# Kernel optimization log

Measured on AMD Instinct MI355X. Metric: run time of the kernel, lower is better.

The kernel has to match this reference:

```python
import jax, jax.numpy as jnp
import numpy as np

N_QUBITS = 12
N_LAYERS = 3
STATE_DIM = 2 ** N_QUBITS  # 4096


def _cnot_perms():
    # Ring of CNOTs: control q -> target (q+1) % n. Qubit 0 is the MSB of the basis index.
    idx = np.arange(STATE_DIM)
    perms = []
    for c in range(N_QUBITS):
        t = (c + 1) % N_QUBITS
        cbit = (idx >> (N_QUBITS - 1 - c)) & 1
        perms.append(np.where(cbit == 1, idx ^ (1 << (N_QUBITS - 1 - t)), idx))
    return np.stack(perms)  # (n_qubits, STATE_DIM), each row an involutive permutation

_CNOT = _cnot_perms()


def _z_signs():
    # sign_q(i) = +1 if bit q of basis index i is 0, else -1
    idx = np.arange(STATE_DIM)
    bits = (idx[None, :] >> (N_QUBITS - 1 - np.arange(N_QUBITS)[:, None])) & 1
    return (1.0 - 2.0 * bits).astype(np.float32)  # (n_qubits, STATE_DIM)

_ZSIGN = jnp.asarray(_z_signs())


def _apply_ry(s, th, q):
    # RY(th) on qubit q, batched over leading dim. RY is real so the state stays real.
    L, R = 2 ** q, 2 ** (N_QUBITS - 1 - q)
    s = s.reshape(-1, L, 2, R)
    c, sn = jnp.cos(th / 2), jnp.sin(th / 2)
    a0 = c * s[:, :, 0, :] - sn * s[:, :, 1, :]
    a1 = sn * s[:, :, 0, :] + c * s[:, :, 1, :]
    return jnp.stack([a0, a1], axis=2).reshape(-1, STATE_DIM)


def _quantum_features(xr, theta):
    # Amplitude encoding: normalize each row to a unit state vector.
    s = xr / (jnp.linalg.norm(xr, axis=1, keepdims=True) + 1e-10)
    for l in range(N_LAYERS):
        for q in range(N_QUBITS):
            s = _apply_ry(s, theta[l, q], q)
        for q in range(N_QUBITS):
            s = s[:, _CNOT[q]]  # CNOT as a static gather permutation
    probs = s * s  # |amplitude|^2 (real state)
    return probs @ _ZSIGN.T  # (B, n_qubits) Pauli-Z expectations


def setup_inputs() -> dict:
    key = jax.random.key(0)
    ks = jax.random.split(key, 9)
    B, F = 8192, 8192
    d = {}
    d["x"] = jax.random.normal(ks[0], (B, F), jnp.float32)
    # feature reducer Linear(F, STATE_DIM)
    d["W_red"] = jax.random.normal(ks[1], (STATE_DIM, F), jnp.float32) / np.sqrt(F).astype(np.float32)
    d["b_red"] = jnp.zeros((STATE_DIM,), jnp.float32)
    # variational RY angles
    d["theta"] = jax.random.normal(ks[2], (N_LAYERS, N_QUBITS), jnp.float32)
    # classical head: n_qubits -> 32 -> 16 -> 1
    d["W1"] = jax.random.normal(ks[3], (32, N_QUBITS), jnp.float32) / np.sqrt(N_QUBITS).astype(np.float32)
    d["b1"] = jnp.zeros((32,), jnp.float32)
    d["W2"] = jax.random.normal(ks[4], (16, 32), jnp.float32) / np.sqrt(32.0).astype(np.float32)
    d["b2"] = jnp.zeros((16,), jnp.float32)
    d["W3"] = jax.random.normal(ks[5], (1, 16), jnp.float32) / 4.0
    d["b3"] = jnp.zeros((1,), jnp.float32)
    return d


def reference(x, W_red, b_red, theta, W1, b1, W2, b2, W3, b3):
    xr = x @ W_red.T + b_red                      # (B, STATE_DIM)
    m = _quantum_features(xr, theta)              # (B, N_QUBITS)
    h = jax.nn.relu(m @ W1.T + b1)                # dropout is identity at inference
    h = jax.nn.relu(h @ W2.T + b2)
    return jax.nn.sigmoid(h @ W3.T + b3)          # (B, 1) risk scores
```

## Files before the change

kernel.cpp:

```cpp
#include <hip/hip_runtime.h>
#include <hip/hip_bf16.h>

#define NQ    12
#define SDIM  4096
#define BATCH 8192
#define FDIM  8192

using bf16x8 = __attribute__((ext_vector_type(8))) short;
using f16x8  = __attribute__((ext_vector_type(8))) _Float16;
using f32x4  = __attribute__((ext_vector_type(4))) float;

__device__ __forceinline__ unsigned short f2bf(float f) {
    unsigned u = __float_as_uint(f);
    u += 0x7FFFu + ((u >> 16) & 1u);
    return (unsigned short)(u >> 16);
}
__device__ __forceinline__ float bf2f(unsigned short h) {
    return __uint_as_float(((unsigned)h) << 16);
}

__device__ __forceinline__ void gl_lds16(const void* g, void* l) {
    __builtin_amdgcn_global_load_lds(
        (const __attribute__((address_space(1))) void*)g,
        (__attribute__((address_space(3))) void*)l, 16, 0, 0);
}

__global__ __launch_bounds__(256)
void cvt_fp16(const float* __restrict__ in, _Float16* __restrict__ out, unsigned n8)
{
    unsigned i = blockIdx.x * 256 + threadIdx.x;
    const unsigned stride = gridDim.x * 256;
    for (; i < n8; i += stride) {
        float4 a = ((const float4*)in)[2 * i];
        float4 b = ((const float4*)in)[2 * i + 1];
        f16x8 o;
        o[0] = (_Float16)a.x; o[1] = (_Float16)a.y; o[2] = (_Float16)a.z; o[3] = (_Float16)a.w;
        o[4] = (_Float16)b.x; o[5] = (_Float16)b.y; o[6] = (_Float16)b.z; o[7] = (_Float16)b.w;
        ((f16x8*)out)[i] = o;
    }
}

__global__ __launch_bounds__(256, 2)
void vqc_gemm_f16(const _Float16* __restrict__ Xh, const _Float16* __restrict__ Wh,
                  const float* __restrict__ bred, _Float16* __restrict__ XR)
{
    __shared__ _Float16 Alds[128 * 64];
    __shared__ _Float16 Blds[128 * 64];

    const int t    = threadIdx.x;
    const int lane = t & 63;
    const int wv   = t >> 6;
    const int wr   = wv >> 1, wc = wv & 1;
    const int l16  = lane & 15, lg = lane >> 4;
    const int bm0  = blockIdx.y * 128;
    const int bn0  = blockIdx.x * 128;
    const int lr   = lane >> 3;
    const int lc   = (lane & 7) * 8;

    f32x4 acc[4][4] = {};

    for (int bk = 0; bk < FDIM; bk += 64) {
        #pragma unroll
        for (int i = 0; i < 4; i++) {
            int r0 = wv * 32 + i * 8;
            gl_lds16(Xh + (size_t)(bm0 + r0 + lr) * FDIM + bk + lc, (char*)Alds + r0 * 128);
            gl_lds16(Wh + (size_t)(bn0 + r0 + lr) * FDIM + bk + lc, (char*)Blds + r0 * 128);
        }
        __syncthreads();
        #pragma unroll
        for (int ks = 0; ks < 2; ks++) {
            f16x8 af[4], bf_[4];
            #pragma unroll
            for (int m = 0; m < 4; m++) {
                int row = wr * 64 + m * 16 + l16;
                af[m] = *(const f16x8*)((const char*)Alds + row * 128 + ks * 64 + lg * 16);
            }
            #pragma unroll
            for (int n = 0; n < 4; n++) {
                int row = wc * 64 + n * 16 + l16;
                bf_[n] = *(const f16x8*)((const char*)Blds + row * 128 + ks * 64 + lg * 16);
            }
            #pragma unroll
            for (int m = 0; m < 4; m++)
                #pragma unroll
                for (int n = 0; n < 4; n++)
                    acc[m][n] = __builtin_amdgcn_mfma_f32_16x16x32_f16(af[m], bf_[n], acc[m][n], 0, 0, 0);
        }
        __syncthreads();
    }
    #pragma unroll
    for (int n = 0; n < 4; n++) {
        int col = bn0 + wc * 64 + n * 16 + l16;
        float bb = bred[col];
        #pragma unroll
        for (int m = 0; m < 4; m++) {
            int rowb = bm0 + wr * 64 + m * 16 + lg * 4;
            #pragma unroll
            for (int j = 0; j < 4; j++)
                XR[(size_t)(rowb + j) * SDIM + col] = (_Float16)(acc[m][n][j] + bb);
        }
    }
}

__global__ __launch_bounds__(256, 2)
void vqc_gemm_split(const float* __restrict__ X, const float* __restrict__ W,
                    const float* __restrict__ bred, float* __restrict__ XR)
{
    __shared__ unsigned char lds[65536];
    unsigned char* Ah = lds;
    unsigned char* Al = lds + 16384;
    unsigned char* Bh = lds + 32768;
    unsigned char* Bl = lds + 49152;

    const int t    = threadIdx.x;
    const int lane = t & 63;
    const int w    = t >> 6;
    const int wr   = w >> 1, wc = w & 1;
    const int bm0  = blockIdx.y * 128;
    const int bn0  = blockIdx.x * 128;
    const int l16  = lane & 15;
    const int lg   = lane >> 4;

    f32x4 acc[4][4] = {};

    for (int bk = 0; bk < FDIM; bk += 64) {
        float4 av[8], bv[8];
        #pragma unroll
        for (int i = 0; i < 8; i++) {
            int p   = i * 256 + t;
            int row = p >> 4, c4 = p & 15;
            av[i] = *(const float4*)(X + (size_t)(bm0 + row) * FDIM + bk + c4 * 4);
            bv[i] = *(const float4*)(W + (size_t)(bn0 + row) * FDIM + bk + c4 * 4);
        }
        __syncthreads();
        #pragma unroll
        for (int i = 0; i < 8; i++) {
            int p   = i * 256 + t;
            int row = p >> 4, c4 = p & 15;
            unsigned addr = ((unsigned)(row * 128 + c4 * 8)) ^ ((unsigned)((row & 7) << 4));
            {
                float4 v = av[i];
                unsigned short h0 = f2bf(v.x), h1 = f2bf(v.y), h2 = f2bf(v.z), h3 = f2bf(v.w);
                unsigned short l0 = f2bf(v.x - bf2f(h0)), l1 = f2bf(v.y - bf2f(h1));
                unsigned short l2 = f2bf(v.z - bf2f(h2)), l3 = f2bf(v.w - bf2f(h3));
                *(uint2*)(Ah + addr) = make_uint2((unsigned)h0 | ((unsigned)h1 << 16),
                                                  (unsigned)h2 | ((unsigned)h3 << 16));
                *(uint2*)(Al + addr) = make_uint2((unsigned)l0 | ((unsigned)l1 << 16),
                                                  (unsigned)l2 | ((unsigned)l3 << 16));
            }
            {
                float4 v = bv[i];
                unsigned short h0 = f2bf(v.x), h1 = f2bf(v.y), h2 = f2bf(v.z), h3 = f2bf(v.w);
                unsigned short l0 = f2bf(v.x - bf2f(h0)), l1 = f2bf(v.y - bf2f(h1));
                unsigned short l2 = f2bf(v.z - bf2f(h2)), l3 = f2bf(v.w - bf2f(h3));
                *(uint2*)(Bh + addr) = make_uint2((unsigned)h0 | ((unsigned)h1 << 16),
                                                  (unsigned)h2 | ((unsigned)h3 << 16));
                *(uint2*)(Bl + addr) = make_uint2((unsigned)l0 | ((unsigned)l1 << 16),
                                                  (unsigned)l2 | ((unsigned)l3 << 16));
            }
        }
        __syncthreads();
        #pragma unroll
        for (int ks = 0; ks < 2; ks++) {
            bf16x8 aH[4], aL[4], bH[4], bL[4];
            const int slot = ks * 4 + lg;
            #pragma unroll
            for (int m = 0; m < 4; m++) {
                int row = wr * 64 + m * 16 + l16;
                unsigned off = ((unsigned)(row * 128 + slot * 16)) ^ ((unsigned)((row & 7) << 4));
                aH[m] = *(const bf16x8*)(Ah + off);
                aL[m] = *(const bf16x8*)(Al + off);
            }
            #pragma unroll
            for (int n = 0; n < 4; n++) {
                int row = wc * 64 + n * 16 + l16;
                unsigned off = ((unsigned)(row * 128 + slot * 16)) ^ ((unsigned)((row & 7) << 4));
                bH[n] = *(const bf16x8*)(Bh + off);
                bL[n] = *(const bf16x8*)(Bl + off);
            }
            #pragma unroll
            for (int m = 0; m < 4; m++)
                #pragma unroll
                for (int n = 0; n < 4; n++) {
                    acc[m][n] = __builtin_amdgcn_mfma_f32_16x16x32_bf16(aH[m], bH[n], acc[m][n], 0, 0, 0);
                    acc[m][n] = __builtin_amdgcn_mfma_f32_16x16x32_bf16(aH[m], bL[n], acc[m][n], 0, 0, 0);
                    acc[m][n] = __builtin_amdgcn_mfma_f32_16x16x32_bf16(aL[m], bH[n], acc[m][n], 0, 0, 0);
                }
        }
    }
    #pragma unroll
    for (int n = 0; n < 4; n++) {
        int col = bn0 + wc * 64 + n * 16 + l16;
        float bb = bred[col];
        #pragma unroll
        for (int m = 0; m < 4; m++) {
            int rowb = bm0 + wr * 64 + m * 16 + lg * 4;
            #pragma unroll
            for (int j = 0; j < 4; j++)
                XR[(size_t)(rowb + j) * SDIM + col] = acc[m][n][j] + bb;
        }
    }
}

template <typename T>
__global__ __launch_bounds__(256)
void vqc_circuit(const T* __restrict__ XR, const float* __restrict__ theta,
                 const float* __restrict__ W1, const float* __restrict__ b1,
                 const float* __restrict__ W2, const float* __restrict__ b2,
                 const float* __restrict__ W3, const float* __restrict__ b3,
                 float* __restrict__ OUT)
{
    __shared__ float s[SDIM];
    __shared__ float cs_[36], sn_[36];
    __shared__ float wred[4];
    __shared__ float mred[48];

    const int t = threadIdx.x;
    const int lane = t & 63;
    const int w = t >> 6;
    const size_t row = blockIdx.x;
    const T* src = XR + row * SDIM;

    if (t < 36) { float th = theta[t] * 0.5f; cs_[t] = cosf(th); sn_[t] = sinf(th); }

    float ss = 0.f;
    if constexpr (sizeof(T) == 2) {
        #pragma unroll
        for (int i = 0; i < 2; i++) {
            f16x8 v = *(const f16x8*)(src + (size_t)(i * 256 + t) * 8);
            float f[8];
            #pragma unroll
            for (int j = 0; j < 8; j++) { f[j] = (float)v[j]; ss += f[j] * f[j]; }
            #pragma unroll
            for (int j = 0; j < 8; j++) s[(i * 256 + t) * 8 + j] = f[j];
        }
    } else {
        #pragma unroll
        for (int i = 0; i < 4; i++) {
            float4 v = *(const float4*)((const float*)src + (size_t)(i * 256 + t) * 4);
            ss += v.x * v.x + v.y * v.y + v.z * v.z + v.w * v.w;
            *(float4*)(s + (i * 256 + t) * 4) = v;
        }
    }
    #pragma unroll
    for (int off = 32; off; off >>= 1) ss += __shfl_down(ss, off);
    if (lane == 0) wred[w] = ss;
    __syncthreads();
    const float scale = 1.f / (sqrtf(wred[0] + wred[1] + wred[2] + wred[3]) + 1e-10f);
    #pragma unroll
    for (int j = 0; j < 16; j++) s[j * 256 + t] *= scale;

    int gperm[16];
    #pragma unroll
    for (int j = 0; j < 16; j++) {
        int p = j * 256 + t;
        #pragma unroll
        for (int q = 11; q >= 0; q--) {
            const int tq = (q + 1) % 12;
            const int cm = 1 << (11 - q);
            const int tm = 1 << (11 - tq);
            if (p & cm) p ^= tm;
        }
        gperm[j] = p;
    }
    __syncthreads();

    for (int l = 0; l < 3; l++) {
        #pragma unroll
        for (int q = 0; q < 12; q++) {
            const float c = cs_[l * 12 + q], sn = sn_[l * 12 + q];
            const int R = 1 << (11 - q);
            #pragma unroll
            for (int j = 0; j < 8; j++) {
                int p  = j * 256 + t;
                int i0 = ((p & ~(R - 1)) << 1) | (p & (R - 1));
                int i1 = i0 | R;
                float a0 = s[i0], a1 = s[i1];
                s[i0] = c * a0 - sn * a1;
                s[i1] = sn * a0 + c * a1;
            }
            __syncthreads();
        }
        float tmp[16];
        #pragma unroll
        for (int j = 0; j < 16; j++) tmp[j] = s[gperm[j]];
        __syncthreads();
        #pragma unroll
        for (int j = 0; j < 16; j++) s[j * 256 + t] = tmp[j];
        __syncthreads();
    }

    float mq[12] = {};
    #pragma unroll
    for (int j = 0; j < 16; j++) {
        int i = j * 256 + t;
        float p = s[i] * s[i];
        #pragma unroll
        for (int q = 0; q < 12; q++)
            mq[q] += ((i >> (11 - q)) & 1) ? -p : p;
    }
    #pragma unroll
    for (int q = 0; q < 12; q++)
        #pragma unroll
        for (int off = 32; off; off >>= 1) mq[q] += __shfl_down(mq[q], off);
    if (lane == 0) {
        #pragma unroll
        for (int q = 0; q < 12; q++) mred[w * 12 + q] = mq[q];
    }
    __syncthreads();

    if (t == 0) {
        float m[12];
        #pragma unroll
        for (int q = 0; q < 12; q++)
            m[q] = mred[q] + mred[12 + q] + mred[24 + q] + mred[36 + q];
        float h1[32];
        for (int k = 0; k < 32; k++) {
            float z = b1[k];
            for (int j = 0; j < 12; j++) z += W1[k * 12 + j] * m[j];
            h1[k] = fmaxf(z, 0.f);
        }
        float h2[16];
        for (int k = 0; k < 16; k++) {
            float z = b2[k];
            for (int j = 0; j < 32; j++) z += W2[k * 32 + j] * h1[j];
            h2[k] = fmaxf(z, 0.f);
        }
        float z = b3[0];
        for (int j = 0; j < 16; j++) z += W3[j] * h2[j];
        OUT[row] = 1.f / (1.f + expf(-z));
    }
}

extern "C" void kernel_launch(void* const* d_in, const int* in_sizes, int n_in,
                              void* d_out, int out_size, void* d_ws, size_t ws_size,
                              hipStream_t stream)
{
    const float* x     = (const float*)d_in[0];
    const float* W_red = (const float*)d_in[1];
    const float* b_red = (const float*)d_in[2];
    const float* theta = (const float*)d_in[3];
    const float* W1    = (const float*)d_in[4];
    const float* b1    = (const float*)d_in[5];
    const float* W2    = (const float*)d_in[6];
    const float* b2    = (const float*)d_in[7];
    const float* W3    = (const float*)d_in[8];
    const float* b3    = (const float*)d_in[9];
    float* out = (float*)d_out;

    const size_t SZ_XH = (size_t)BATCH * FDIM * 2;
    const size_t SZ_WH = (size_t)SDIM * FDIM * 2;
    const size_t SZ_XR = (size_t)BATCH * SDIM * 2;
    const size_t NEED  = SZ_XH + SZ_WH + SZ_XR;

    if (ws_size >= NEED) {
        _Float16* Xh = (_Float16*)d_ws;
        _Float16* Wh = (_Float16*)((char*)d_ws + SZ_XH);
        _Float16* xr = (_Float16*)((char*)d_ws + SZ_XH + SZ_WH);
        cvt_fp16<<<2048, 256, 0, stream>>>(x, Xh, (unsigned)((size_t)BATCH * FDIM / 8));
        cvt_fp16<<<1024, 256, 0, stream>>>(W_red, Wh, (unsigned)((size_t)SDIM * FDIM / 8));
        dim3 g1(SDIM / 128, BATCH / 128);
        vqc_gemm_f16<<<g1, 256, 0, stream>>>(Xh, Wh, b_red, xr);
        vqc_circuit<_Float16><<<BATCH, 256, 0, stream>>>(xr, theta, W1, b1, W2, b2, W3, b3, out);
    } else {
        float* xr = (float*)d_ws;
        dim3 g1(SDIM / 128, BATCH / 128);
        vqc_gemm_split<<<g1, 256, 0, stream>>>(x, W_red, b_red, xr);
        vqc_circuit<float><<<BATCH, 256, 0, stream>>>(xr, theta, W1, b1, W2, b2, W3, b3, out);
    }
}
```

Measured before the change: 1.386 ms.

## Swizzle GEMM LDS tiles and keep quantum state in registers with shuffles

The GEMM now XOR-swizzles the 16-byte chunks of the A/B LDS tiles by row, to cut LDS bank conflicts on the MFMA fragment reads. The quantum-circuit kernel now holds each thread's 16 amplitudes in registers. The top four qubits are applied in-register, qubits 4–5 through one LDS exchange, and qubits 6–11 with wave shuffles. This replaces twelve LDS read/write passes, each followed by a barrier, in every layer. The CNOT permutation is read back from LDS straight into registers. The costs are more register use and a more intricate index mapping.

```diff
diff --git a/kernel.cpp b/kernel.cpp
--- a/kernel.cpp
+++ b/kernel.cpp
@@ -55,7 +55,7 @@
     const int bm0  = blockIdx.y * 128;
     const int bn0  = blockIdx.x * 128;
     const int lr   = lane >> 3;
-    const int lc   = (lane & 7) * 8;
+    const int lcsw = ((lane & 7) ^ lr) * 8;
 
     f32x4 acc[4][4] = {};
 
@@ -63,8 +63,8 @@
         #pragma unroll
         for (int i = 0; i < 4; i++) {
             int r0 = wv * 32 + i * 8;
-            gl_lds16(Xh + (size_t)(bm0 + r0 + lr) * FDIM + bk + lc, (char*)Alds + r0 * 128);
-            gl_lds16(Wh + (size_t)(bn0 + r0 + lr) * FDIM + bk + lc, (char*)Blds + r0 * 128);
+            gl_lds16(Xh + (size_t)(bm0 + r0 + lr) * FDIM + bk + lcsw, (char*)Alds + r0 * 128);
+            gl_lds16(Wh + (size_t)(bn0 + r0 + lr) * FDIM + bk + lcsw, (char*)Blds + r0 * 128);
         }
         __syncthreads();
         #pragma unroll
@@ -73,12 +73,14 @@
             #pragma unroll
             for (int m = 0; m < 4; m++) {
                 int row = wr * 64 + m * 16 + l16;
-                af[m] = *(const f16x8*)((const char*)Alds + row * 128 + ks * 64 + lg * 16);
+                unsigned off = ((unsigned)(row * 128 + ks * 64 + lg * 16)) ^ ((unsigned)((row & 7) << 4));
+                af[m] = *(const f16x8*)((const char*)Alds + off);
             }
             #pragma unroll
             for (int n = 0; n < 4; n++) {
                 int row = wc * 64 + n * 16 + l16;
-                bf_[n] = *(const f16x8*)((const char*)Blds + row * 128 + ks * 64 + lg * 16);
+                unsigned off = ((unsigned)(row * 128 + ks * 64 + lg * 16)) ^ ((unsigned)((row & 7) << 4));
+                bf_[n] = *(const f16x8*)((const char*)Blds + off);
             }
             #pragma unroll
             for (int m = 0; m < 4; m++)
@@ -223,24 +225,12 @@
 
     if (t < 36) { float th = theta[t] * 0.5f; cs_[t] = cosf(th); sn_[t] = sinf(th); }
 
+    float v[16];
     float ss = 0.f;
-    if constexpr (sizeof(T) == 2) {
-        #pragma unroll
-        for (int i = 0; i < 2; i++) {
-            f16x8 v = *(const f16x8*)(src + (size_t)(i * 256 + t) * 8);
-            float f[8];
-            #pragma unroll
-            for (int j = 0; j < 8; j++) { f[j] = (float)v[j]; ss += f[j] * f[j]; }
-            #pragma unroll
-            for (int j = 0; j < 8; j++) s[(i * 256 + t) * 8 + j] = f[j];
-        }
-    } else {
-        #pragma unroll
-        for (int i = 0; i < 4; i++) {
-            float4 v = *(const float4*)((const float*)src + (size_t)(i * 256 + t) * 4);
-            ss += v.x * v.x + v.y * v.y + v.z * v.z + v.w * v.w;
-            *(float4*)(s + (i * 256 + t) * 4) = v;
-        }
+    #pragma unroll
+    for (int j = 0; j < 16; j++) {
+        v[j] = (float)src[j * 256 + t];
+        ss += v[j] * v[j];
     }
     #pragma unroll
     for (int off = 32; off; off >>= 1) ss += __shfl_down(ss, off);
@@ -248,9 +238,9 @@
     __syncthreads();
     const float scale = 1.f / (sqrtf(wred[0] + wred[1] + wred[2] + wred[3]) + 1e-10f);
     #pragma unroll
-    for (int j = 0; j < 16; j++) s[j * 256 + t] *= scale;
-
-    int gperm[16];
+    for (int j = 0; j < 16; j++) v[j] *= scale;
+
+    int gp[16];
     #pragma unroll
     for (int j = 0; j < 16; j++) {
         int p = j * 256 + t;
@@ -261,40 +251,69 @@
             const int tm = 1 << (11 - tq);
             if (p & cm) p ^= tm;
         }
-        gperm[j] = p;
-    }
-    __syncthreads();
+        gp[j] = p;
+    }
+
+    const bool ax4 = (t & 128) != 0;
+    const bool ax5 = (t & 64) != 0;
 
     for (int l = 0; l < 3; l++) {
-        #pragma unroll
-        for (int q = 0; q < 12; q++) {
-            const float c = cs_[l * 12 + q], sn = sn_[l * 12 + q];
-            const int R = 1 << (11 - q);
-            #pragma unroll
-            for (int j = 0; j < 8; j++) {
-                int p  = j * 256 + t;
-                int i0 = ((p & ~(R - 1)) << 1) | (p & (R - 1));
-                int i1 = i0 | R;
-                float a0 = s[i0], a1 = s[i1];
-                s[i0] = c * a0 - sn * a1;
-                s[i1] = sn * a0 + c * a1;
-            }
-            __syncthreads();
-        }
-        float tmp[16];
-        #pragma unroll
-        for (int j = 0; j < 16; j++) tmp[j] = s[gperm[j]];
-        __syncthreads();
-        #pragma unroll
-        for (int j = 0; j < 16; j++) s[j * 256 + t] = tmp[j];
-        __syncthreads();
+        const int lb = l * 12;
+        #pragma unroll
+        for (int g = 0; g < 4; g++) {
+            const int m = 8 >> g;
+            const float c = cs_[lb + g], sp = sn_[lb + g];
+            float nv[16];
+            #pragma unroll
+            for (int j = 0; j < 16; j++) {
+                float sg = (j & m) ? sp : -sp;
+                nv[j] = fmaf(sg, v[j ^ m], c * v[j]);
+            }
+            #pragma unroll
+            for (int j = 0; j < 16; j++) v[j] = nv[j];
+        }
+        __syncthreads();
+        #pragma unroll
+        for (int j = 0; j < 16; j++) s[j * 256 + t] = v[j];
+        __syncthreads();
+        {
+            const float c4 = cs_[lb + 4], s4 = ax4 ? sn_[lb + 4] : -sn_[lb + 4];
+            const float c5 = cs_[lb + 5], s5 = ax5 ? sn_[lb + 5] : -sn_[lb + 5];
+            const int pA = t ^ 128, pB = t ^ 64, pAB = t ^ 192;
+            #pragma unroll
+            for (int j = 0; j < 16; j++) {
+                float vA  = s[j * 256 + pA];
+                float vB  = s[j * 256 + pB];
+                float vAB = s[j * 256 + pAB];
+                float w_me = fmaf(s4, vA,  c4 * v[j]);
+                float w_bf = fmaf(s4, vAB, c4 * vB);
+                v[j] = fmaf(s5, w_bf, c5 * w_me);
+            }
+        }
+        #pragma unroll
+        for (int g = 6; g < 12; g++) {
+            const int R = 1 << (11 - g);
+            const float c = cs_[lb + g];
+            const float sg = (t & R) ? sn_[lb + g] : -sn_[lb + g];
+            #pragma unroll
+            for (int j = 0; j < 16; j++) {
+                float vp = __shfl_xor(v[j], R);
+                v[j] = fmaf(sg, vp, c * v[j]);
+            }
+        }
+        __syncthreads();
+        #pragma unroll
+        for (int j = 0; j < 16; j++) s[j * 256 + t] = v[j];
+        __syncthreads();
+        #pragma unroll
+        for (int j = 0; j < 16; j++) v[j] = s[gp[j]];
     }
 
     float mq[12] = {};
     #pragma unroll
     for (int j = 0; j < 16; j++) {
-        int i = j * 256 + t;
-        float p = s[i] * s[i];
+        const int i = j * 256 + t;
+        float p = v[j] * v[j];
         #pragma unroll
         for (int q = 0; q < 12; q++)
             mq[q] += ((i >> (11 - q)) & 1) ? -p : p;
```

New measurement: 1.184 ms. -14.6%, faster.
